# Kernel tuning notes

Measured on AMD Instinct MI355X. Metric: run time of the kernel, lower is better.

## Reference

```python
import jax, jax.numpy as jnp
import numpy as np

B, T, S = 512, 2048, 24
START, STOP = 22, 23
NEG = -10000.0


def setup_inputs() -> dict:
    key = jax.random.key(0)
    k1, k2, k3, k4 = jax.random.split(key, 4)
    feats = jax.random.normal(k1, (B, T, S), dtype=jnp.float32)
    transitions = jax.random.normal(k2, (S, S), dtype=jnp.float32)
    # match torch __init__: no transition INTO START, none OUT OF STOP
    transitions = transitions.at[START, :].set(NEG).at[:, STOP].set(NEG)
    tags = jax.random.randint(k3, (B, T), 0, START)          # gold tags exclude START/STOP
    lengths = jax.random.randint(k4, (B,), 1, T + 1)         # true lengths in [1, T]
    return {"feats": feats, "transitions": transitions, "tags": tags, "lengths": lengths}


def reference(feats, transitions, tags, lengths):
    Bb, Tt, Ss = feats.shape
    mask = jnp.arange(Tt)[None, :] < lengths[:, None]  # (B, T) valid-step mask

    # ---- forward algorithm (log partition) ----
    init = jnp.full((Bb, Ss), NEG, dtype=feats.dtype).at[:, START].set(0.0)

    def step(fv, xs):
        feat_t, m_t = xs  # (B, S), (B,)
        # score[b, next, prev] = fv[b, prev] + trans[next, prev]; logsumexp over prev
        nxt = jax.nn.logsumexp(fv[:, None, :] + transitions[None, :, :], axis=2) + feat_t
        fv_new = jnp.where(m_t[:, None], nxt, fv)
        return fv_new, None

    fv, _ = jax.lax.scan(step, init, (feats.transpose(1, 0, 2), mask.T))
    alpha = jax.nn.logsumexp(fv + transitions[STOP][None, :], axis=1)  # (B,)

    # ---- gold sequence score ----
    start_col = jnp.full((Bb, 1), START, dtype=tags.dtype)
    ext = jnp.concatenate([start_col, tags], axis=1)  # (B, T+1)
    cur, prev = ext[:, 1:], ext[:, :-1]
    trans_s = transitions[cur, prev]                                  # (B, T)
    emit_s = jnp.take_along_axis(feats, cur[:, :, None], axis=2)[..., 0]  # (B, T)
    last_tags = jnp.take_along_axis(tags, (lengths - 1)[:, None], axis=1)[:, 0]
    gold = jnp.sum(jnp.where(mask, trans_s + emit_s, 0.0), axis=1) + transitions[STOP, last_tags]

    return jnp.mean(alpha - gold)
```

## Files before the change

### kernel.cpp

```cpp
#include <hip/hip_runtime.h>
#include <math.h>

#define NBATCH 512
#define TLEN   2048
#define NS     24
#define KSTART 22
#define KSTOP  23
#define MID    1024
#define L2E    1.4426950408889634f
#define LN2F   0.6931471805599453f

#define GOLD_CHUNKS 4
#define GOLD_CLEN   (TLEN / GOLD_CHUNKS)
#define WS_TOTAL    (NBATCH + NBATCH * GOLD_CHUNKS)

__device__ __forceinline__ float fexp2(float x) {
#if __has_builtin(__builtin_amdgcn_exp2f)
  return __builtin_amdgcn_exp2f(x);
#else
  return exp2f(x);
#endif
}
__device__ __forceinline__ float flog2(float x) {
#if __has_builtin(__builtin_amdgcn_logf)
  return __builtin_amdgcn_logf(x);
#else
  return __log2f(x);
#endif
}

__device__ __forceinline__ float rl(float v, int k) {
  return __int_as_float(__builtin_amdgcn_readlane(__float_as_int(v), k));
}

#define SWZ(X, IMM) __int_as_float(__builtin_amdgcn_ds_swizzle(__float_as_int(X), (IMM)))

template<bool ISB>
__device__ __forceinline__ void run_chain(
    const float* __restrict__ fb, const float* __restrict__ trans,
    int steps, int lenm1, int j, int je,
    float* __restrict__ outg, float* __restrict__ outc)
{
  const bool act = (j < NS);

  float p[NS];
  #pragma unroll
  for (int k = 0; k < NS; ++k) {
    int idx = ISB ? (k * NS + je) : (je * NS + k);
    float tv = trans[idx];
    p[k] = act ? fexp2(tv * L2E) : 0.0f;
  }

  float g;
  if (ISB) g = act ? fexp2(trans[KSTOP * NS + je] * L2E) : 0.0f;
  else     g = (j == KSTART) ? 1.0f : 0.0f;
  int cE = 0;

  auto ldf = [&](int k) -> float {
    int t = ISB ? (lenm1 - k) : k;
    t = (t < 0) ? 0 : t;
    return fb[t * NS + je];
  };

#define DOT24(SRC) \
  const float s0  = rl(SRC, 0),  s1  = rl(SRC, 1),  s2  = rl(SRC, 2),  s3  = rl(SRC, 3),  \
              s4  = rl(SRC, 4),  s5  = rl(SRC, 5),  s6  = rl(SRC, 6),  s7  = rl(SRC, 7),  \
              s8  = rl(SRC, 8),  s9  = rl(SRC, 9),  s10 = rl(SRC, 10), s11 = rl(SRC, 11), \
              s12 = rl(SRC, 12), s13 = rl(SRC, 13), s14 = rl(SRC, 14), s15 = rl(SRC, 15), \
              s16 = rl(SRC, 16), s17 = rl(SRC, 17), s18 = rl(SRC, 18), s19 = rl(SRC, 19), \
              s20 = rl(SRC, 20), s21 = rl(SRC, 21), s22 = rl(SRC, 22), s23 = rl(SRC, 23); \
  y0 = p[0] * s0;              y1 = p[1] * s1;              y2 = p[2] * s2;              y3 = p[3] * s3; \
  y0 = fmaf(p[4],  s4,  y0);   y1 = fmaf(p[5],  s5,  y1);   y2 = fmaf(p[6],  s6,  y2);   y3 = fmaf(p[7],  s7,  y3); \
  y0 = fmaf(p[8],  s8,  y0);   y1 = fmaf(p[9],  s9,  y1);   y2 = fmaf(p[10], s10, y2);   y3 = fmaf(p[11], s11, y3); \
  y0 = fmaf(p[12], s12, y0);   y1 = fmaf(p[13], s13, y1);   y2 = fmaf(p[14], s14, y2);   y3 = fmaf(p[15], s15, y3); \
  y0 = fmaf(p[16], s16, y0);   y1 = fmaf(p[17], s17, y1);   y2 = fmaf(p[18], s18, y2);   y3 = fmaf(p[19], s19, y3); \
  y0 = fmaf(p[20], s20, y0);   y1 = fmaf(p[21], s21, y1);   y2 = fmaf(p[22], s22, y2);   y3 = fmaf(p[23], s23, y3);

#define STEP1(EU) { float y0, y1, y2, y3; \
    if constexpr (ISB) { float m = g * (EU); DOT24(m); g = (y0 + y1) + (y2 + y3); } \
    else               { DOT24(g); g = ((y0 + y1) + (y2 + y3)) * (EU); } }

#define RENORM { int b0_ = __builtin_amdgcn_readlane(__float_as_int(g), 0); \
    int er_ = (b0_ >> 23) & 0xFF; int E_ = (er_ == 0) ? 0 : (er_ - 127); \
    cE += E_; g *= __int_as_float((127 - E_) << 23); }

  float f0 = ldf(0), f1 = ldf(1), f2 = ldf(2), f3 = ldf(3),
        f4 = ldf(4), f5 = ldf(5), f6 = ldf(6), f7 = ldf(7);
  float e0 = fexp2(f0 * L2E), e1 = fexp2(f1 * L2E), e2 = fexp2(f2 * L2E), e3 = fexp2(f3 * L2E),
        e4 = fexp2(f4 * L2E), e5 = fexp2(f5 * L2E), e6 = fexp2(f6 * L2E), e7 = fexp2(f7 * L2E);
  f0 = ldf(8);  f1 = ldf(9);  f2 = ldf(10); f3 = ldf(11);
  f4 = ldf(12); f5 = ldf(13); f6 = ldf(14); f7 = ldf(15);

  int k0 = 0;
  for (; k0 + 8 <= steps; k0 += 8) {
    float n0 = ldf(k0 + 16), n1 = ldf(k0 + 17), n2 = ldf(k0 + 18), n3 = ldf(k0 + 19),
          n4 = ldf(k0 + 20), n5 = ldf(k0 + 21), n6 = ldf(k0 + 22), n7 = ldf(k0 + 23);
    float x0 = fexp2(f0 * L2E), x1 = fexp2(f1 * L2E), x2 = fexp2(f2 * L2E), x3 = fexp2(f3 * L2E),
          x4 = fexp2(f4 * L2E), x5 = fexp2(f5 * L2E), x6 = fexp2(f6 * L2E), x7 = fexp2(f7 * L2E);
    STEP1(e0) STEP1(e1) STEP1(e2) STEP1(e3)
    RENORM
    STEP1(e4) STEP1(e5) STEP1(e6) STEP1(e7)
    RENORM
    f0 = n0; f1 = n1; f2 = n2; f3 = n3; f4 = n4; f5 = n5; f6 = n6; f7 = n7;
    e0 = x0; e1 = x1; e2 = x2; e3 = x3; e4 = x4; e5 = x5; e6 = x6; e7 = x7;
  }
  int r = steps - k0;
  if (r > 0) STEP1(e0)
  if (r > 1) STEP1(e1)
  if (r > 2) STEP1(e2)
  if (r > 3) STEP1(e3)
  if (r > 4) { RENORM STEP1(e4) }
  if (r > 5) STEP1(e5)
  if (r > 6) STEP1(e6)
  RENORM

  if (act) outg[j] = g;
  if (j == 0) *outc = (float)cE;

#undef DOT24
#undef STEP1
#undef RENORM
}

__global__ __launch_bounds__(128) __attribute__((amdgpu_waves_per_eu(1, 2)))
void crf_chains(
    const float* __restrict__ feats, const float* __restrict__ trans,
    const int* __restrict__ lengths, float* __restrict__ ws)
{
  __shared__ float shg[2][NS];
  __shared__ float shc[2];
  const int b   = blockIdx.x;
  const int tid = threadIdx.x;
  const int dir = tid >> 6;
  const int j   = tid & 63;
  const int je  = (j < NS) ? j : (NS - 1);
  const int len = lengths[b];
  const int lenm1 = len - 1;
  const float* fb = feats + (size_t)b * (TLEN * NS);

  if (dir == 0) {
    int fsteps = (len < MID) ? len : MID;
    run_chain<false>(fb, trans, fsteps, lenm1, j, je, shg[0], &shc[0]);
  } else {
    int bsteps = (len > MID) ? (len - MID) : 0;
    run_chain<true>(fb, trans, bsteps, lenm1, j, je, shg[1], &shc[1]);
  }
  __syncthreads();

  if (tid < 32) {
    float prod = (tid < NS) ? shg[0][tid] * shg[1][tid] : 0.0f;
    prod += SWZ(prod, 0x041F);
    prod += SWZ(prod, 0x081F);
    prod += SWZ(prod, 0x101F);
    prod += SWZ(prod, 0x201F);
    prod += SWZ(prod, 0x401F);
    if (tid == 0) {
      float alpha2 = shc[0] + shc[1] + flog2(prod);
      ws[b] = alpha2 * LN2F;
    }
  }
}

__global__ __launch_bounds__(256) void crf_gold(
    const float* __restrict__ feats, const float* __restrict__ trans,
    const int* __restrict__ tags, const int* __restrict__ lengths,
    float* __restrict__ ws)
{
  const int blk = blockIdx.x;
  const int b   = blk >> 2;
  const int c   = blk & 3;
  const int tid = threadIdx.x;
  const int len = lengths[b];
  const int* tg = tags + (size_t)b * TLEN;
  const float* fb = feats + (size_t)b * (TLEN * NS);

  const int t0 = c * GOLD_CLEN + tid;
  const int t1 = t0 + 256;

  float s = 0.0f;
  if (t0 < len) {
    int cur  = tg[t0];
    int prev = (t0 == 0) ? KSTART : tg[t0 - 1];
    s += trans[cur * NS + prev] + fb[t0 * NS + cur];
  }
  if (t1 < len) {
    int cur  = tg[t1];
    int prev = tg[t1 - 1];
    s += trans[cur * NS + prev] + fb[t1 * NS + cur];
  }
  if (c == 0 && tid == 0) s += trans[KSTOP * NS + tg[len - 1]];

  __shared__ float red[256];
  red[tid] = s;
  __syncthreads();
  for (int off = 128; off > 0; off >>= 1) {
    if (tid < off) red[tid] += red[tid + off];
    __syncthreads();
  }
  if (tid == 0) ws[NBATCH + blk] = -red[0];
}

__global__ __launch_bounds__(256) void crf_final(const float* __restrict__ ws,
                                                 float* __restrict__ out)
{
  const int tid = threadIdx.x;
  float s = 0.0f;
  for (int i = tid; i < WS_TOTAL; i += 256) s += ws[i];
  __shared__ float red[256];
  red[tid] = s;
  __syncthreads();
  for (int off = 128; off > 0; off >>= 1) {
    if (tid < off) red[tid] += red[tid + off];
    __syncthreads();
  }
  if (tid == 0) out[0] = red[0] * (1.0f / (float)NBATCH);
}

extern "C" void kernel_launch(void* const* d_in, const int* in_sizes, int n_in,
                              void* d_out, int out_size, void* d_ws, size_t ws_size,
                              hipStream_t stream) {
  const float* feats   = (const float*)d_in[0];
  const float* trans   = (const float*)d_in[1];
  const int*   tags    = (const int*)d_in[2];
  const int*   lengths = (const int*)d_in[3];
  float* out = (float*)d_out;
  float* ws  = (float*)d_ws;

  crf_chains<<<NBATCH, 128, 0, stream>>>(feats, trans, lengths, ws);
  crf_gold<<<NBATCH * GOLD_CHUNKS, 256, 0, stream>>>(feats, trans, tags, lengths, ws);
  crf_final<<<1, 256, 0, stream>>>(ws, out);
}
```

Baseline: 331.6 us.

## Fuse gold-score computation into idle lanes of the chain kernel

Removes the separate gold-path kernel and computes the gold sequence score in the otherwise idle upper 32 lanes of each chain wavefront. Those loads are software-pipelined across the recurrence loop. The feature prefetch distance is deepened from two to three groups of eight steps, and a sched_barrier is added between readlanes and FMAs. This removes one launch and the extra pass over feats/tags, at the cost of more registers and instructions in the latency-critical serial loop.

```diff
diff --git a/kernel.cpp b/kernel.cpp
--- a/kernel.cpp
+++ b/kernel.cpp
@@ -10,10 +10,6 @@
 #define L2E    1.4426950408889634f
 #define LN2F   0.6931471805599453f
 
-#define GOLD_CHUNKS 4
-#define GOLD_CLEN   (TLEN / GOLD_CHUNKS)
-#define WS_TOTAL    (NBATCH + NBATCH * GOLD_CHUNKS)
-
 __device__ __forceinline__ float fexp2(float x) {
 #if __has_builtin(__builtin_amdgcn_exp2f)
   return __builtin_amdgcn_exp2f(x);
@@ -38,8 +34,10 @@
 template<bool ISB>
 __device__ __forceinline__ void run_chain(
     const float* __restrict__ fb, const float* __restrict__ trans,
-    int steps, int lenm1, int j, int je,
-    float* __restrict__ outg, float* __restrict__ outc)
+    const int* __restrict__ tg,
+    int steps, int lenm1, int lane, int j, int je,
+    float* __restrict__ outg, float* __restrict__ outc,
+    float* __restrict__ sgold, int dir)
 {
   const bool act = (j < NS);
 
@@ -61,6 +59,30 @@
     t = (t < 0) ? 0 : t;
     return fb[t * NS + je];
   };
+
+  const int li  = lane - 32;
+  const int T0_ = ISB ? MID : 0;
+  const unsigned R_ = (unsigned)steps;
+  int   tcA = 0, tpA = 0, tcB = 0, tpB = 0, tcC = 0, tpC = 0;
+  float fvA = 0.f, fvB = 0.f, fvC = 0.f, tvA = 0.f, tvB = 0.f, tvC = 0.f;
+  float gs = 0.f;
+
+#define GOLDG(GG) \
+  if (lane >= 32) { \
+    fvC = fvB; fvB = fvA; tvC = tvB; tvB = tvA; \
+    tcC = tcB; tcB = tcA; tpC = tpB; tpB = tpA; \
+    unsigned vq_ = (unsigned)(32 * ((GG) - 4) + li); \
+    if (vq_ < R_) gs += fvC + tvC; \
+    int tq_  = T0_ + 32 * ((GG) - 2) + li; \
+    int tqc_ = (tq_ < 0) ? 0 : ((tq_ > lenm1) ? lenm1 : tq_); \
+    int cur_ = tcC, prev_ = (tq_ == 0) ? KSTART : tpC; \
+    fvA = fb[tqc_ * NS + cur_]; \
+    tvA = trans[cur_ * NS + prev_]; \
+    int t0_  = T0_ + 32 * (GG) + li; \
+    int t0c_ = (t0_ > lenm1) ? lenm1 : t0_; \
+    tcA = tg[t0c_]; \
+    tpA = tg[(t0c_ > 0) ? (t0c_ - 1) : 0]; \
+  }
 
 #define DOT24(SRC) \
   const float s0  = rl(SRC, 0),  s1  = rl(SRC, 1),  s2  = rl(SRC, 2),  s3  = rl(SRC, 3),  \
@@ -69,6 +91,7 @@
               s12 = rl(SRC, 12), s13 = rl(SRC, 13), s14 = rl(SRC, 14), s15 = rl(SRC, 15), \
               s16 = rl(SRC, 16), s17 = rl(SRC, 17), s18 = rl(SRC, 18), s19 = rl(SRC, 19), \
               s20 = rl(SRC, 20), s21 = rl(SRC, 21), s22 = rl(SRC, 22), s23 = rl(SRC, 23); \
+  __builtin_amdgcn_sched_barrier(0); \
   y0 = p[0] * s0;              y1 = p[1] * s1;              y2 = p[2] * s2;              y3 = p[3] * s3; \
   y0 = fmaf(p[4],  s4,  y0);   y1 = fmaf(p[5],  s5,  y1);   y2 = fmaf(p[6],  s6,  y2);   y3 = fmaf(p[7],  s7,  y3); \
   y0 = fmaf(p[8],  s8,  y0);   y1 = fmaf(p[9],  s9,  y1);   y2 = fmaf(p[10], s10, y2);   y3 = fmaf(p[11], s11, y3); \
@@ -84,25 +107,35 @@
     int er_ = (b0_ >> 23) & 0xFF; int E_ = (er_ == 0) ? 0 : (er_ - 127); \
     cE += E_; g *= __int_as_float((127 - E_) << 23); }
 
-  float f0 = ldf(0), f1 = ldf(1), f2 = ldf(2), f3 = ldf(3),
-        f4 = ldf(4), f5 = ldf(5), f6 = ldf(6), f7 = ldf(7);
-  float e0 = fexp2(f0 * L2E), e1 = fexp2(f1 * L2E), e2 = fexp2(f2 * L2E), e3 = fexp2(f3 * L2E),
-        e4 = fexp2(f4 * L2E), e5 = fexp2(f5 * L2E), e6 = fexp2(f6 * L2E), e7 = fexp2(f7 * L2E);
-  f0 = ldf(8);  f1 = ldf(9);  f2 = ldf(10); f3 = ldf(11);
-  f4 = ldf(12); f5 = ldf(13); f6 = ldf(14); f7 = ldf(15);
-
+  float e0, e1, e2, e3, e4, e5, e6, e7;
+  float rb0, rb1, rb2, rb3, rb4, rb5, rb6, rb7;
+  float rc0, rc1, rc2, rc3, rc4, rc5, rc6, rc7;
+  {
+    float a0 = ldf(0), a1 = ldf(1), a2 = ldf(2), a3 = ldf(3),
+          a4 = ldf(4), a5 = ldf(5), a6 = ldf(6), a7 = ldf(7);
+    rb0 = ldf(8);  rb1 = ldf(9);  rb2 = ldf(10); rb3 = ldf(11);
+    rb4 = ldf(12); rb5 = ldf(13); rb6 = ldf(14); rb7 = ldf(15);
+    rc0 = ldf(16); rc1 = ldf(17); rc2 = ldf(18); rc3 = ldf(19);
+    rc4 = ldf(20); rc5 = ldf(21); rc6 = ldf(22); rc7 = ldf(23);
+    e0 = fexp2(a0 * L2E); e1 = fexp2(a1 * L2E); e2 = fexp2(a2 * L2E); e3 = fexp2(a3 * L2E);
+    e4 = fexp2(a4 * L2E); e5 = fexp2(a5 * L2E); e6 = fexp2(a6 * L2E); e7 = fexp2(a7 * L2E);
+  }
+
+  int gi = 0;
   int k0 = 0;
-  for (; k0 + 8 <= steps; k0 += 8) {
-    float n0 = ldf(k0 + 16), n1 = ldf(k0 + 17), n2 = ldf(k0 + 18), n3 = ldf(k0 + 19),
-          n4 = ldf(k0 + 20), n5 = ldf(k0 + 21), n6 = ldf(k0 + 22), n7 = ldf(k0 + 23);
-    float x0 = fexp2(f0 * L2E), x1 = fexp2(f1 * L2E), x2 = fexp2(f2 * L2E), x3 = fexp2(f3 * L2E),
-          x4 = fexp2(f4 * L2E), x5 = fexp2(f5 * L2E), x6 = fexp2(f6 * L2E), x7 = fexp2(f7 * L2E);
+  for (; k0 + 8 <= steps; k0 += 8, ++gi) {
+    float rn0 = ldf(k0 + 24), rn1 = ldf(k0 + 25), rn2 = ldf(k0 + 26), rn3 = ldf(k0 + 27),
+          rn4 = ldf(k0 + 28), rn5 = ldf(k0 + 29), rn6 = ldf(k0 + 30), rn7 = ldf(k0 + 31);
+    GOLDG(gi)
+    float x0 = fexp2(rb0 * L2E), x1 = fexp2(rb1 * L2E), x2 = fexp2(rb2 * L2E), x3 = fexp2(rb3 * L2E),
+          x4 = fexp2(rb4 * L2E), x5 = fexp2(rb5 * L2E), x6 = fexp2(rb6 * L2E), x7 = fexp2(rb7 * L2E);
     STEP1(e0) STEP1(e1) STEP1(e2) STEP1(e3)
     RENORM
     STEP1(e4) STEP1(e5) STEP1(e6) STEP1(e7)
     RENORM
-    f0 = n0; f1 = n1; f2 = n2; f3 = n3; f4 = n4; f5 = n5; f6 = n6; f7 = n7;
     e0 = x0; e1 = x1; e2 = x2; e3 = x3; e4 = x4; e5 = x5; e6 = x6; e7 = x7;
+    rb0 = rc0; rb1 = rc1; rb2 = rc2; rb3 = rc3; rb4 = rc4; rb5 = rc5; rb6 = rc6; rb7 = rc7;
+    rc0 = rn0; rc1 = rn1; rc2 = rn2; rc3 = rn3; rc4 = rn4; rc5 = rn5; rc6 = rn6; rc7 = rn7;
   }
   int r = steps - k0;
   if (r > 0) STEP1(e0)
@@ -114,9 +147,15 @@
   if (r > 6) STEP1(e6)
   RENORM
 
+  for (int gd = 0; gd < 5; ++gd, ++gi) {
+    GOLDG(gi)
+  }
+
   if (act) outg[j] = g;
   if (j == 0) *outc = (float)cE;
-
+  if (lane >= 32) sgold[(dir << 5) + li] = gs;
+
+#undef GOLDG
 #undef DOT24
 #undef STEP1
 #undef RENORM
@@ -125,79 +164,47 @@
 __global__ __launch_bounds__(128) __attribute__((amdgpu_waves_per_eu(1, 2)))
 void crf_chains(
     const float* __restrict__ feats, const float* __restrict__ trans,
-    const int* __restrict__ lengths, float* __restrict__ ws)
+    const int* __restrict__ tags, const int* __restrict__ lengths,
+    float* __restrict__ ws)
 {
   __shared__ float shg[2][NS];
   __shared__ float shc[2];
+  __shared__ float sgold[64];
   const int b   = blockIdx.x;
   const int tid = threadIdx.x;
   const int dir = tid >> 6;
-  const int j   = tid & 63;
+  const int lane = tid & 63;
+  const int j   = lane;
   const int je  = (j < NS) ? j : (NS - 1);
   const int len = lengths[b];
   const int lenm1 = len - 1;
   const float* fb = feats + (size_t)b * (TLEN * NS);
+  const int*   tg = tags  + (size_t)b * TLEN;
+
+  const int ltag = tg[lenm1];
 
   if (dir == 0) {
     int fsteps = (len < MID) ? len : MID;
-    run_chain<false>(fb, trans, fsteps, lenm1, j, je, shg[0], &shc[0]);
+    run_chain<false>(fb, trans, tg, fsteps, lenm1, lane, j, je, shg[0], &shc[0], sgold, 0);
   } else {
     int bsteps = (len > MID) ? (len - MID) : 0;
-    run_chain<true>(fb, trans, bsteps, lenm1, j, je, shg[1], &shc[1]);
+    run_chain<true>(fb, trans, tg, bsteps, lenm1, lane, j, je, shg[1], &shc[1], sgold, 1);
   }
   __syncthreads();
 
   if (tid < 32) {
     float prod = (tid < NS) ? shg[0][tid] * shg[1][tid] : 0.0f;
-    prod += SWZ(prod, 0x041F);
-    prod += SWZ(prod, 0x081F);
-    prod += SWZ(prod, 0x101F);
-    prod += SWZ(prod, 0x201F);
-    prod += SWZ(prod, 0x401F);
+    float gtot = sgold[tid] + sgold[tid + 32];
+    prod += SWZ(prod, 0x041F);  gtot += SWZ(gtot, 0x041F);
+    prod += SWZ(prod, 0x081F);  gtot += SWZ(gtot, 0x081F);
+    prod += SWZ(prod, 0x101F);  gtot += SWZ(gtot, 0x101F);
+    prod += SWZ(prod, 0x201F);  gtot += SWZ(gtot, 0x201F);
+    prod += SWZ(prod, 0x401F);  gtot += SWZ(gtot, 0x401F);
     if (tid == 0) {
       float alpha2 = shc[0] + shc[1] + flog2(prod);
-      ws[b] = alpha2 * LN2F;
+      ws[b] = alpha2 * LN2F - (gtot + trans[KSTOP * NS + ltag]);
     }
   }
-}
-
-__global__ __launch_bounds__(256) void crf_gold(
-    const float* __restrict__ feats, const float* __restrict__ trans,
-    const int* __restrict__ tags, const int* __restrict__ lengths,
-    float* __restrict__ ws)
-{
-  const int blk = blockIdx.x;
-  const int b   = blk >> 2;
-  const int c   = blk & 3;
-  const int tid = threadIdx.x;
-  const int len = lengths[b];
-  const int* tg = tags + (size_t)b * TLEN;
-  const float* fb = feats + (size_t)b * (TLEN * NS);
-
-  const int t0 = c * GOLD_CLEN + tid;
-  const int t1 = t0 + 256;
-
-  float s = 0.0f;
-  if (t0 < len) {
-    int cur  = tg[t0];
-    int prev = (t0 == 0) ? KSTART : tg[t0 - 1];
-    s += trans[cur * NS + prev] + fb[t0 * NS + cur];
-  }
-  if (t1 < len) {
-    int cur  = tg[t1];
-    int prev = tg[t1 - 1];
-    s += trans[cur * NS + prev] + fb[t1 * NS + cur];
-  }
-  if (c == 0 && tid == 0) s += trans[KSTOP * NS + tg[len - 1]];
-
-  __shared__ float red[256];
-  red[tid] = s;
-  __syncthreads();
-  for (int off = 128; off > 0; off >>= 1) {
-    if (tid < off) red[tid] += red[tid + off];
-    __syncthreads();
-  }
-  if (tid == 0) ws[NBATCH + blk] = -red[0];
 }
 
 __global__ __launch_bounds__(256) void crf_final(const float* __restrict__ ws,
@@ -205,7 +212,7 @@
 {
   const int tid = threadIdx.x;
   float s = 0.0f;
-  for (int i = tid; i < WS_TOTAL; i += 256) s += ws[i];
+  for (int i = tid; i < NBATCH; i += 256) s += ws[i];
   __shared__ float red[256];
   red[tid] = s;
   __syncthreads();
@@ -226,7 +233,6 @@
   float* out = (float*)d_out;
   float* ws  = (float*)d_ws;
 
-  crf_chains<<<NBATCH, 128, 0, stream>>>(feats, trans, lengths, ws);
-  crf_gold<<<NBATCH * GOLD_CHUNKS, 256, 0, stream>>>(feats, trans, tags, lengths, ws);
+  crf_chains<<<NBATCH, 128, 0, stream>>>(feats, trans, tags, lengths, ws);
   crf_final<<<1, 256, 0, stream>>>(ws, out);
 }
```

New measurement: 346.3 us. +4.4%, slower.
